# Performance work log

Measured on AMD Instinct MI355X. Metric: run time of the kernel, lower is better.

Reference implementation:

```python
import jax, jax.numpy as jnp
import numpy as np

N_NODES = 100000
N_EDGES = 1600000
N_GRAPHS = 1024
EMB = 32
HID = 64
N_CLASSES = 10
N_SHAPE = 16
N_COLOR = 8


def setup_inputs() -> dict:
    key = jax.random.key(0)
    ks = jax.random.split(key, 12)
    shape_id = jax.random.randint(ks[0], (N_NODES,), 0, N_SHAPE + 1, dtype=jnp.int32)
    color_id = jax.random.randint(ks[1], (N_NODES,), 0, N_COLOR + 1, dtype=jnp.int32)
    edge_index = jax.random.randint(ks[2], (2, N_EDGES), 0, N_NODES, dtype=jnp.int32)
    batch = jnp.sort(jax.random.randint(ks[3], (N_NODES,), 0, N_GRAPHS, dtype=jnp.int32))
    shape_table = jax.random.normal(ks[4], (N_SHAPE + 1, EMB), jnp.float32)
    color_table = jax.random.normal(ks[5], (N_COLOR + 1, EMB), jnp.float32)
    W1 = jax.random.normal(ks[6], (EMB, HID), jnp.float32) / np.sqrt(EMB)
    b1 = jnp.zeros((HID,), jnp.float32)
    W2 = jax.random.normal(ks[7], (HID, HID), jnp.float32) / np.sqrt(HID)
    b2 = jnp.zeros((HID,), jnp.float32)
    Wl = jax.random.normal(ks[8], (HID, N_CLASSES), jnp.float32) / np.sqrt(HID)
    bl = jnp.zeros((N_CLASSES,), jnp.float32)
    return dict(shape_id=shape_id, color_id=color_id, edge_index=edge_index, batch=batch,
                shape_table=shape_table, color_table=color_table,
                W1=W1, b1=b1, W2=W2, b2=b2, Wl=Wl, bl=bl)


def gcn_conv(x, W, b, src, dst, num_nodes):
    # PyG GCNConv: add self-loops, symmetric normalization D^-1/2 (A+I) D^-1/2
    h = x @ W  # [N, out]
    deg = 1.0 + jax.ops.segment_sum(jnp.ones_like(dst, jnp.float32), dst, num_segments=num_nodes)
    dis = jax.lax.rsqrt(deg)  # deg >= 1 due to self-loop
    norm = dis[src] * dis[dst]  # [E]
    agg = jax.ops.segment_sum(h[src] * norm[:, None], dst, num_segments=num_nodes)
    agg = agg + h * (dis * dis)[:, None]  # self-loop term
    return agg + b


def reference(shape_id, color_id, edge_index, batch, shape_table, color_table,
              W1, b1, W2, b2, Wl, bl):
    # padding_idx=0 -> row 0 contributes zeros
    st = shape_table.at[0].set(0.0)
    ct = color_table.at[0].set(0.0)
    x = st[shape_id] + ct[color_id]  # [N, emb]
    src, dst = edge_index[0], edge_index[1]
    x = jax.nn.relu(gcn_conv(x, W1, b1, src, dst, N_NODES))
    x = jax.nn.relu(gcn_conv(x, W2, b2, src, dst, N_NODES))
    # global_mean_pool over batch ids
    sums = jax.ops.segment_sum(x, batch, num_segments=N_GRAPHS)
    cnts = jax.ops.segment_sum(jnp.ones((x.shape[0],), x.dtype), batch, num_segments=N_GRAPHS)
    pooled = sums / jnp.maximum(cnts, 1.0)[:, None]  # [B, hidden]
    return pooled @ Wl + bl  # [B, num_classes]
```

## Files before the change

kernel.cpp:

```cpp
#include <hip/hip_runtime.h>
#include <hip/hip_bf16.h>
#include <hip/hip_fp16.h>

#define N_NODES   100000
#define N_EDGES   1600000
#define N_GRAPHS  1024
#define EMB       32
#define HID       64
#define N_CLASSES 10
#define SCAN_BLOCKS 391
#define NCOMBO 153
#define BUCK_NODES 448
#define NBUCK 224
#define BIN_CAP 8192
#define EPB 4096

typedef _Float16 f16x8 __attribute__((ext_vector_type(8)));
typedef float f32x4 __attribute__((ext_vector_type(4)));

__global__ __launch_bounds__(256) void prep_kernel(
    const int* __restrict__ sid, const int* __restrict__ cid,
    const int* __restrict__ batch, int* __restrict__ combo, int* __restrict__ gstart) {
    int v = blockIdx.x * 256 + threadIdx.x;
    if (v < N_NODES) {
        combo[v] = sid[v] * 9 + cid[v];
        int b = batch[v];
        int bp = (v == 0) ? -1 : batch[v - 1];
        for (int g = bp + 1; g <= b; ++g) gstart[g] = v;
        if (v == N_NODES - 1) {
            for (int g = b + 1; g <= N_GRAPHS; ++g) gstart[g] = N_NODES;
        }
    }
}

__global__ __launch_bounds__(64) void tc_kernel(
    const float* __restrict__ st, const float* __restrict__ ct,
    const float* __restrict__ W1, __half* __restrict__ TCh) {
    int r = blockIdx.x, j = threadIdx.x;
    int s = r / 9, c = r % 9;
    float acc = 0.0f;
    if (s != 0) {
#pragma unroll
        for (int k = 0; k < EMB; ++k) acc = fmaf(st[s * EMB + k], W1[k * HID + j], acc);
    }
    if (c != 0) {
#pragma unroll
        for (int k = 0; k < EMB; ++k) acc = fmaf(ct[c * EMB + k], W1[k * HID + j], acc);
    }
    TCh[r * HID + j] = __float2half_rn(acc);
}

__global__ __launch_bounds__(512) void binA_kernel(
    const int* __restrict__ src, const int* __restrict__ dst,
    const int* __restrict__ combo, int* __restrict__ gcur,
    int2* __restrict__ gbin) {
    __shared__ int2 stg[EPB];
    __shared__ int hist[NBUCK];
    __shared__ int base[NBUCK + 1];
    __shared__ int gstart[NBUCK];
    __shared__ int scanbuf[256];
    int t = threadIdx.x;
    int e0 = blockIdx.x * EPB;
    for (int i = t; i < NBUCK; i += 512) hist[i] = 0;
    __syncthreads();

    int2 myq[8];
    int mybo[8];
#pragma unroll
    for (int i = 0; i < 8; ++i) {
        int e = e0 + t + i * 512;
        if (e < N_EDGES) {
            int d = dst[e];
            int s = src[e];
            unsigned b = (unsigned)d / BUCK_NODES;
            int off = atomicAdd(&hist[b], 1);
            myq[i].x = s | (combo[s] << 17);
            myq[i].y = d;
            mybo[i] = (int)(b << 16) | off;
        } else {
            mybo[i] = -1;
        }
    }
    __syncthreads();

    int h = (t < NBUCK) ? hist[t] : 0;
    if (t < 256) scanbuf[t] = h;
    __syncthreads();
#pragma unroll
    for (int off = 1; off < 256; off <<= 1) {
        int x = (t < 256 && t >= off) ? scanbuf[t - off] : 0;
        __syncthreads();
        if (t < 256) scanbuf[t] += x;
        __syncthreads();
    }
    if (t < NBUCK) base[t] = scanbuf[t] - h;
    if (t == 0) base[NBUCK] = scanbuf[255];
    __syncthreads();
#pragma unroll
    for (int i = 0; i < 8; ++i) {
        if (mybo[i] >= 0) {
            int b = mybo[i] >> 16, off = mybo[i] & 0xFFFF;
            stg[base[b] + off] = myq[i];
        }
    }
    if (t < NBUCK) {
        int n = hist[t];
        gstart[t] = n ? atomicAdd(&gcur[t], n) : 0;
    }
    __syncthreads();
    int total = base[NBUCK];
    for (int i = t; i < total; i += 512) {
        int2 q = stg[i];
        unsigned b = (unsigned)q.y / BUCK_NODES;
        gbin[(size_t)b * BIN_CAP + gstart[b] + (i - base[b])] = q;
    }
}

__global__ __launch_bounds__(256) void bscan_kernel(const int* __restrict__ gcur,
                                                    int* __restrict__ bktbase) {
    __shared__ int s[256];
    int t = threadIdx.x;
    int g = (t < NBUCK) ? gcur[t] : 0;
    s[t] = g; __syncthreads();
#pragma unroll
    for (int off = 1; off < 256; off <<= 1) {
        int x = (t >= off) ? s[t - off] : 0;
        __syncthreads();
        s[t] += x;
        __syncthreads();
    }
    if (t < NBUCK) bktbase[t] = s[t] - g;
}

__global__ __launch_bounds__(512) void bucket_kernel(
    const int2* __restrict__ gbin, const int* __restrict__ gcur,
    const int* __restrict__ bktbase, float* __restrict__ dis,
    int* __restrict__ rowptr) {
    __shared__ int ldeg[BUCK_NODES];
    __shared__ int s[512];
    int b = blockIdx.x, t = threadIdx.x;
    for (int i = t; i < BUCK_NODES; i += 512) ldeg[i] = 0;
    __syncthreads();
    int n = gcur[b];
    const int2* mybin = gbin + (size_t)b * BIN_CAP;
    for (int i = t; i < n; i += 512)
        atomicAdd(&ldeg[mybin[i].y - b * BUCK_NODES], 1);
    __syncthreads();
    int d = (t < BUCK_NODES) ? ldeg[t] : 0;
    int v = b * BUCK_NODES + t;
    if (t < BUCK_NODES && v < N_NODES) dis[v] = rsqrtf(1.0f + (float)d);
    s[t] = d;
    __syncthreads();
#pragma unroll
    for (int off = 1; off < 512; off <<= 1) {
        int x = (t >= off) ? s[t - off] : 0;
        __syncthreads();
        s[t] += x;
        __syncthreads();
    }
    if (t < BUCK_NODES && v < N_NODES) rowptr[v] = bktbase[b] + s[t] - d;
    if (b == 0 && t == 0) rowptr[N_NODES] = N_EDGES;
}

__global__ __launch_bounds__(1024) void binB_kernel(
    const int2* __restrict__ gbin, const int* __restrict__ gcur,
    const int* __restrict__ rowptr, const float* __restrict__ dis,
    int2* __restrict__ epack) {
    __shared__ int curs[BUCK_NODES];
    int b = blockIdx.x, t = threadIdx.x;
    for (int i = t; i < BUCK_NODES; i += 1024) curs[i] = 0;
    __syncthreads();
    int n = gcur[b];
    const int2* mybin = gbin + (size_t)b * BIN_CAP;
    for (int i = t; i < n; i += 1024) {
        int2 q = mybin[i];
        int local = q.y - b * BUCK_NODES;
        int r = atomicAdd(&curs[local], 1);
        unsigned sx = (unsigned)q.x;
        int srci = (int)(sx & 0x1FFFF);
        int comboOff = (int)((sx >> 17) * 128u);
        int2 rec;
        rec.x = (srci << 15) | comboOff;
        rec.y = __float_as_int(dis[srci]);
        epack[rowptr[q.y] + r] = rec;
    }
}

#define AGG_CHUNK(Q, LBASE, J0)                                                \
    _Pragma("unroll")                                                          \
    for (int i = 0; i < 8; ++i) {                                              \
        int off = __builtin_amdgcn_readlane((Q).x, (LBASE) + i) & 0x7FFF;      \
        int wb  = __builtin_amdgcn_readlane((Q).y, (LBASE) + i);               \
        off = ((J0) + i < cnt) ? off : 0;                                      \
        wb  = ((J0) + i < cnt) ? wb  : 0;                                      \
        __half tv = *(const __half*)((const char*)TCs + (off + lane2));        \
        acc = fmaf(__int_as_float(wb), __half2float(tv), acc);                 \
    }

#define AGG_NODE(N, RS, RE, DV, CO)                                            \
    {                                                                          \
        int deg = (RE) - (RS);                                                 \
        int cnt = deg > 32 ? 32 : deg;                                         \
        float acc = 0.0f;                                                      \
        AGG_CHUNK(q1, (N)*16, 0)                                               \
        if (cnt > 8)  { AGG_CHUNK(q1, (N)*16 + 8, 8) }                         \
        if (cnt > 16) { AGG_CHUNK(q2, (N)*16, 16) }                            \
        if (cnt > 24) { AGG_CHUNK(q2, (N)*16 + 8, 24) }                        \
        if (deg > 32) {                                                        \
            for (int e = (RS) + 32; e < (RE); ++e) {                           \
                int2 q = epack[e];                                             \
                __half tv = *(const __half*)((const char*)TCs +                \
                                             ((q.x & 0x7FFF) + lane2));        \
                acc = fmaf(__int_as_float(q.y), __half2float(tv), acc);        \
            }                                                                  \
        }                                                                      \
        __half hv = *(const __half*)((const char*)TCs + ((CO) + lane2));       \
        float val = (DV) * fmaf(__half2float(hv), (DV), acc) + bias;           \
        val = val > 0.0f ? val : 0.0f;                                         \
        xsA[w * 4 + (N)][lane] = __float2half_rn(val * (DV));                  \
    }

__global__ __launch_bounds__(256, 6) void agg1_mm2_kernel(
    const int2* __restrict__ epack, const int* __restrict__ rowptr,
    const int* __restrict__ combo, const float* __restrict__ dis,
    const __half* __restrict__ TCh, const float* __restrict__ W2,
    const float* __restrict__ b1, __half* __restrict__ h2s) {
    __shared__ __align__(16) __half TCs[NCOMBO * HID];
    __shared__ __align__(16) __half xsA[16][72];
    __shared__ __align__(16) __half Dst[16 * 64];
    int t = threadIdx.x;
    int lane = t & 63, w = t >> 6;
    int lane2 = lane * 2;
    int vb = blockIdx.x * 16;
    int v0 = vb + w * 4;

    int sub = lane >> 4, sl = lane & 15;
    int rb = rowptr[v0 + sub];
    int2 q1 = epack[rb + sl];
    int2 q2 = epack[rb + 16 + sl];

    int r0 = __builtin_amdgcn_readfirstlane(rowptr[v0]);
    int r1 = __builtin_amdgcn_readfirstlane(rowptr[v0 + 1]);
    int r2 = __builtin_amdgcn_readfirstlane(rowptr[v0 + 2]);
    int r3 = __builtin_amdgcn_readfirstlane(rowptr[v0 + 3]);
    int r4 = __builtin_amdgcn_readfirstlane(rowptr[v0 + 4]);

    float d0 = dis[v0], d1 = dis[v0 + 1], d2 = dis[v0 + 2], d3 = dis[v0 + 3];
    int o0 = combo[v0] << 7, o1 = combo[v0 + 1] << 7;
    int o2 = combo[v0 + 2] << 7, o3 = combo[v0 + 3] << 7;
    float bias = b1[lane];

    f16x8 bf0, bf1;
    {
        int colw = (w << 4) + (lane & 15);
        int kb = (lane >> 4) * 8;
#pragma unroll
        for (int i = 0; i < 8; ++i) {
            bf0[i] = (_Float16)W2[(kb + i) * HID + colw];
            bf1[i] = (_Float16)W2[(32 + kb + i) * HID + colw];
        }
    }

    {
        const int4* s4 = (const int4*)TCh;
        int4* dd4 = (int4*)TCs;
        for (int i = t; i < NCOMBO * HID * 2 / 16; i += 256) dd4[i] = s4[i];
    }
    __syncthreads();

    AGG_NODE(0, r0, r1, d0, o0)
    AGG_NODE(1, r1, r2, d1, o1)
    AGG_NODE(2, r2, r3, d2, o2)
    AGG_NODE(3, r3, r4, d3, o3)

    __syncthreads();

    const __half* xa = &xsA[lane & 15][0];
    f16x8 a0 = *(const f16x8*)(xa + (lane >> 4) * 8);
    f16x8 a1 = *(const f16x8*)(xa + 32 + (lane >> 4) * 8);
    f32x4 dacc = {0.0f, 0.0f, 0.0f, 0.0f};
    dacc = __builtin_amdgcn_mfma_f32_16x16x32_f16(a0, bf0, dacc, 0, 0, 0);
    dacc = __builtin_amdgcn_mfma_f32_16x16x32_f16(a1, bf1, dacc, 0, 0, 0);

    {
        int colg = (w << 4) + (lane & 15);
#pragma unroll
        for (int i = 0; i < 4; ++i)
            Dst[((lane >> 4) * 4 + i) * 64 + colg] = __float2half_rn(dacc[i]);
    }
    __syncthreads();

    {
        const uint2* ds2 = (const uint2*)Dst;
        uint2* go = (uint2*)(h2s + (size_t)vb * HID);
        go[t] = ds2[t];
    }
}

__device__ __forceinline__ float agg2_node(const int* __restrict__ epackx, int sx,
                                           int rs, int re, int lane, int lane2,
                                           const __half* __restrict__ h2s) {
    float acc = 0.0f;
    int p = rs;
    for (;;) {
        int avail = re - p;
        int cnt = avail > 64 ? 64 : avail;
        int vo = (int)((((unsigned)sx) >> 15) << 7);
        int j = 0;
        for (; j + 8 <= cnt; j += 8) {
            float g[8];
#pragma unroll
            for (int i = 0; i < 8; ++i) {
                int off = __builtin_amdgcn_readlane(vo, j + i);
                g[i] = __half2float(*(const __half*)((const char*)h2s + (off + lane2)));
            }
#pragma unroll
            for (int i = 0; i < 8; ++i) acc += g[i];
        }
        if (j < cnt) {
#pragma unroll
            for (int i = 0; i < 8; ++i) {
                int jj = j + i;
                int off = __builtin_amdgcn_readlane(vo, jj & 63);
                float gv = __half2float(*(const __half*)((const char*)h2s + (off + lane2)));
                acc += (jj < cnt) ? gv : 0.0f;
            }
        }
        p += 64;
        if (p >= re) break;
        int idx = p + lane;
        idx = idx < N_EDGES ? idx : N_EDGES - 1;
        sx = epackx[idx * 2];
    }
    return acc;
}

__global__ __launch_bounds__(256, 8) void agg2_pool_kernel(
    const int2* __restrict__ epack, const int* __restrict__ rowptr,
    const __half* __restrict__ h2s, const float* __restrict__ dis,
    const float* __restrict__ b2, const int* __restrict__ batch,
    float* __restrict__ pooled) {
    int t = threadIdx.x, lane = t & 63, w = t >> 6;
    int lane2 = lane * 2;
    const int* epackx = (const int*)epack;
    int v0 = (blockIdx.x * 4 + w) * 4;

    int r0 = __builtin_amdgcn_readfirstlane(rowptr[v0]);
    int r1 = __builtin_amdgcn_readfirstlane(rowptr[v0 + 1]);
    int r2 = __builtin_amdgcn_readfirstlane(rowptr[v0 + 2]);
    int r3 = __builtin_amdgcn_readfirstlane(rowptr[v0 + 3]);
    int r4 = __builtin_amdgcn_readfirstlane(rowptr[v0 + 4]);

    int ia = r0 + lane; ia = ia < N_EDGES ? ia : N_EDGES - 1;
    int ib = r1 + lane; ib = ib < N_EDGES ? ib : N_EDGES - 1;
    int ic = r2 + lane; ic = ic < N_EDGES ? ic : N_EDGES - 1;
    int id = r3 + lane; id = id < N_EDGES ? id : N_EDGES - 1;
    int sa = epackx[ia * 2];
    int sb = epackx[ib * 2];
    int sc = epackx[ic * 2];
    int sd = epackx[id * 2];

    float bv = b2[lane];
    float acc0 = agg2_node(epackx, sa, r0, r1, lane, lane2, h2s);
    float acc1 = agg2_node(epackx, sb, r1, r2, lane, lane2, h2s);
    float acc2 = agg2_node(epackx, sc, r2, r3, lane, lane2, h2s);
    float acc3 = agg2_node(epackx, sd, r3, r4, lane, lane2, h2s);

#define AGG2_VAL(V, ACC, OUT)                                                  \
    {                                                                          \
        float dv = dis[V];                                                     \
        float self = __half2float(h2s[(size_t)(V) * HID + lane]);              \
        float val = dv * ((ACC) + self) + bv;                                  \
        OUT = val > 0.0f ? val : 0.0f;                                         \
    }
    float val0, val1, val2, val3;
    AGG2_VAL(v0, acc0, val0)
    AGG2_VAL(v0 + 1, acc1, val1)
    AGG2_VAL(v0 + 2, acc2, val2)
    AGG2_VAL(v0 + 3, acc3, val3)
#undef AGG2_VAL

    int g0 = __builtin_amdgcn_readfirstlane(batch[v0]);
    int g1 = __builtin_amdgcn_readfirstlane(batch[v0 + 1]);
    int g2 = __builtin_amdgcn_readfirstlane(batch[v0 + 2]);
    int g3 = __builtin_amdgcn_readfirstlane(batch[v0 + 3]);
    float s = val0; int g = g0;
    if (g1 == g) { s += val1; } else { unsafeAtomicAdd(&pooled[g * HID + lane], s); g = g1; s = val1; }
    if (g2 == g) { s += val2; } else { unsafeAtomicAdd(&pooled[g * HID + lane], s); g = g2; s = val2; }
    if (g3 == g) { s += val3; } else { unsafeAtomicAdd(&pooled[g * HID + lane], s); g = g3; s = val3; }
    unsafeAtomicAdd(&pooled[g * HID + lane], s);
}

__global__ __launch_bounds__(64) void logits_kernel(
    const float* __restrict__ pooled, const int* __restrict__ gstart,
    const float* __restrict__ Wl, const float* __restrict__ bl,
    float* __restrict__ out) {
    __shared__ float row[HID];
    int g = blockIdx.x, t = threadIdx.x;
    int c = gstart[g + 1] - gstart[g]; if (c < 1) c = 1;
    row[t] = pooled[g * HID + t] / (float)c;
    __syncthreads();
    if (t < N_CLASSES) {
        float acc = bl[t];
#pragma unroll
        for (int k = 0; k < HID; ++k) acc = fmaf(row[k], Wl[k * N_CLASSES + t], acc);
        out[g * N_CLASSES + t] = acc;
    }
}

extern "C" void kernel_launch(void* const* d_in, const int* in_sizes, int n_in,
                              void* d_out, int out_size, void* d_ws, size_t ws_size,
                              hipStream_t stream) {
    const int*   shape_id = (const int*)d_in[0];
    const int*   color_id = (const int*)d_in[1];
    const int*   edge_idx = (const int*)d_in[2];
    const int*   batch    = (const int*)d_in[3];
    const float* st       = (const float*)d_in[4];
    const float* ct       = (const float*)d_in[5];
    const float* W1       = (const float*)d_in[6];
    const float* b1       = (const float*)d_in[7];
    const float* W2       = (const float*)d_in[8];
    const float* b2       = (const float*)d_in[9];
    const float* Wl       = (const float*)d_in[10];
    const float* bl       = (const float*)d_in[11];
    float* out = (float*)d_out;

    const int* src = edge_idx;
    const int* dst = edge_idx + N_EDGES;

    char* ws = (char*)d_ws;
    int*    combo   = (int*)   (ws + 0);
    float*  dis     = (float*) (ws + 400384);
    int*    bktbase = (int*)   (ws + 800768);
    int*    gstart  = (int*)   (ws + 801792);
    int*    rowptr  = (int*)   (ws + 1201152);
    __half* TCh     = (__half*)(ws + 1603584);
    float*  pooled  = (float*) (ws + 1623552);
    int*    gcur    = (int*)   (ws + 1889792);
    int2*   epack   = (int2*)  (ws + 1890816);
    int2*   gbin    = (int2*)  (ws + 14690816);
    __half* h2s     = (__half*)(ws + 29370880);

    hipMemsetAsync(pooled, 0, N_GRAPHS * HID * sizeof(float), stream);
    hipMemsetAsync(gcur, 0, NBUCK * sizeof(int), stream);

    prep_kernel<<<SCAN_BLOCKS, 256, 0, stream>>>(shape_id, color_id, batch, combo, gstart);

    tc_kernel<<<NCOMBO, 64, 0, stream>>>(st, ct, W1, TCh);

    binA_kernel<<<(N_EDGES + EPB - 1) / EPB, 512, 0, stream>>>(src, dst, combo, gcur, gbin);

    bscan_kernel<<<1, 256, 0, stream>>>(gcur, bktbase);

    bucket_kernel<<<NBUCK, 512, 0, stream>>>(gbin, gcur, bktbase, dis, rowptr);

    binB_kernel<<<NBUCK, 1024, 0, stream>>>(gbin, gcur, rowptr, dis, epack);

    agg1_mm2_kernel<<<6250, 256, 0, stream>>>(epack, rowptr, combo, dis, TCh, W2, b1, h2s);

    agg2_pool_kernel<<<6250, 256, 0, stream>>>(epack, rowptr, h2s, dis, b2, batch, pooled);

    logits_kernel<<<N_GRAPHS, 64, 0, stream>>>(pooled, gstart, Wl, bl, out);
}
```

Baseline: 200.3 us.

## Split edge bins into SoA, fold bucket scan into bucket kernel, pair agg2 nodes

After: 205.2 us. +2.4%, slower.

```diff
diff --git a/kernel.cpp b/kernel.cpp
--- a/kernel.cpp
+++ b/kernel.cpp
@@ -53,7 +53,7 @@
 __global__ __launch_bounds__(512) void binA_kernel(
     const int* __restrict__ src, const int* __restrict__ dst,
     const int* __restrict__ combo, int* __restrict__ gcur,
-    int2* __restrict__ gbin) {
+    int* __restrict__ gbinx, int* __restrict__ gbiny) {
     __shared__ int2 stg[EPB];
     __shared__ int hist[NBUCK];
     __shared__ int base[NBUCK + 1];
@@ -112,39 +112,34 @@
     for (int i = t; i < total; i += 512) {
         int2 q = stg[i];
         unsigned b = (unsigned)q.y / BUCK_NODES;
-        gbin[(size_t)b * BIN_CAP + gstart[b] + (i - base[b])] = q;
-    }
-}
-
-__global__ __launch_bounds__(256) void bscan_kernel(const int* __restrict__ gcur,
-                                                    int* __restrict__ bktbase) {
-    __shared__ int s[256];
-    int t = threadIdx.x;
-    int g = (t < NBUCK) ? gcur[t] : 0;
-    s[t] = g; __syncthreads();
-#pragma unroll
-    for (int off = 1; off < 256; off <<= 1) {
-        int x = (t >= off) ? s[t - off] : 0;
-        __syncthreads();
-        s[t] += x;
-        __syncthreads();
-    }
-    if (t < NBUCK) bktbase[t] = s[t] - g;
+        size_t pos = (size_t)b * BIN_CAP + gstart[b] + (i - base[b]);
+        gbinx[pos] = q.x;
+        gbiny[pos] = q.y;
+    }
 }
 
 __global__ __launch_bounds__(512) void bucket_kernel(
-    const int2* __restrict__ gbin, const int* __restrict__ gcur,
-    const int* __restrict__ bktbase, float* __restrict__ dis,
-    int* __restrict__ rowptr) {
+    const int* __restrict__ gbiny, const int* __restrict__ gcur,
+    float* __restrict__ dis, int* __restrict__ rowptr) {
     __shared__ int ldeg[BUCK_NODES];
     __shared__ int s[512];
+    __shared__ int sc[256];
     int b = blockIdx.x, t = threadIdx.x;
+    if (t < 256) sc[t] = (t < NBUCK) ? gcur[t] : 0;
     for (int i = t; i < BUCK_NODES; i += 512) ldeg[i] = 0;
     __syncthreads();
+#pragma unroll
+    for (int off = 1; off < 256; off <<= 1) {
+        int x = (t < 256 && t >= off) ? sc[t - off] : 0;
+        __syncthreads();
+        if (t < 256) sc[t] += x;
+        __syncthreads();
+    }
+    int bb = (b == 0) ? 0 : sc[b - 1];
     int n = gcur[b];
-    const int2* mybin = gbin + (size_t)b * BIN_CAP;
+    const int* mybin = gbiny + (size_t)b * BIN_CAP;
     for (int i = t; i < n; i += 512)
-        atomicAdd(&ldeg[mybin[i].y - b * BUCK_NODES], 1);
+        atomicAdd(&ldeg[mybin[i] - b * BUCK_NODES], 1);
     __syncthreads();
     int d = (t < BUCK_NODES) ? ldeg[t] : 0;
     int v = b * BUCK_NODES + t;
@@ -158,12 +153,13 @@
         s[t] += x;
         __syncthreads();
     }
-    if (t < BUCK_NODES && v < N_NODES) rowptr[v] = bktbase[b] + s[t] - d;
+    if (t < BUCK_NODES && v < N_NODES) rowptr[v] = bb + s[t] - d;
     if (b == 0 && t == 0) rowptr[N_NODES] = N_EDGES;
 }
 
 __global__ __launch_bounds__(1024) void binB_kernel(
-    const int2* __restrict__ gbin, const int* __restrict__ gcur,
+    const int* __restrict__ gbinx, const int* __restrict__ gbiny,
+    const int* __restrict__ gcur,
     const int* __restrict__ rowptr, const float* __restrict__ dis,
     int2* __restrict__ epack) {
     __shared__ int curs[BUCK_NODES];
@@ -171,18 +167,20 @@
     for (int i = t; i < BUCK_NODES; i += 1024) curs[i] = 0;
     __syncthreads();
     int n = gcur[b];
-    const int2* mybin = gbin + (size_t)b * BIN_CAP;
+    const int* mx = gbinx + (size_t)b * BIN_CAP;
+    const int* my = gbiny + (size_t)b * BIN_CAP;
     for (int i = t; i < n; i += 1024) {
-        int2 q = mybin[i];
-        int local = q.y - b * BUCK_NODES;
+        int qx = mx[i];
+        int qy = my[i];
+        int local = qy - b * BUCK_NODES;
         int r = atomicAdd(&curs[local], 1);
-        unsigned sx = (unsigned)q.x;
+        unsigned sx = (unsigned)qx;
         int srci = (int)(sx & 0x1FFFF);
         int comboOff = (int)((sx >> 17) * 128u);
         int2 rec;
         rec.x = (srci << 15) | comboOff;
         rec.y = __float_as_int(dis[srci]);
-        epack[rowptr[q.y] + r] = rec;
+        epack[rowptr[qy] + r] = rec;
     }
 }
 
@@ -297,45 +295,58 @@
     }
 }
 
-__device__ __forceinline__ float agg2_node(const int* __restrict__ epackx, int sx,
-                                           int rs, int re, int lane, int lane2,
-                                           const __half* __restrict__ h2s) {
-    float acc = 0.0f;
-    int p = rs;
-    for (;;) {
-        int avail = re - p;
-        int cnt = avail > 64 ? 64 : avail;
-        int vo = (int)((((unsigned)sx) >> 15) << 7);
-        int j = 0;
-        for (; j + 8 <= cnt; j += 8) {
-            float g[8];
+__device__ __forceinline__ void agg2_pair(
+    const int* __restrict__ epackx, const __half* __restrict__ h2s,
+    int sxA, int rsA, int reA, int sxB, int rsB, int reB,
+    int lane2, float* outA, float* outB) {
+    int degA = reA - rsA, degB = reB - rsB;
+    int cntA = degA > 64 ? 64 : degA;
+    int cntB = degB > 64 ? 64 : degB;
+    int voA = (int)(((unsigned)sxA >> 15) << 7);
+    int voB = (int)(((unsigned)sxB >> 15) << 7);
+    float aA = 0.0f, aB = 0.0f;
+    int cmax = cntA > cntB ? cntA : cntB;
+    for (int j = 0; j < cmax; j += 8) {
+        float gA[8], gB[8];
+        bool dA = j < cntA, dB = j < cntB;
+        if (dA) {
 #pragma unroll
             for (int i = 0; i < 8; ++i) {
-                int off = __builtin_amdgcn_readlane(vo, j + i);
-                g[i] = __half2float(*(const __half*)((const char*)h2s + (off + lane2)));
+                int off = __builtin_amdgcn_readlane(voA, (j + i) & 63);
+                float v = __half2float(*(const __half*)((const char*)h2s + (off + lane2)));
+                gA[i] = (j + i < cntA) ? v : 0.0f;
             }
-#pragma unroll
-            for (int i = 0; i < 8; ++i) acc += g[i];
-        }
-        if (j < cnt) {
+        }
+        if (dB) {
 #pragma unroll
             for (int i = 0; i < 8; ++i) {
-                int jj = j + i;
-                int off = __builtin_amdgcn_readlane(vo, jj & 63);
-                float gv = __half2float(*(const __half*)((const char*)h2s + (off + lane2)));
-                acc += (jj < cnt) ? gv : 0.0f;
+                int off = __builtin_amdgcn_readlane(voB, (j + i) & 63);
+                float v = __half2float(*(const __half*)((const char*)h2s + (off + lane2)));
+                gB[i] = (j + i < cntB) ? v : 0.0f;
             }
         }
-        p += 64;
-        if (p >= re) break;
-        int idx = p + lane;
-        idx = idx < N_EDGES ? idx : N_EDGES - 1;
-        sx = epackx[idx * 2];
-    }
-    return acc;
-}
-
-__global__ __launch_bounds__(256, 8) void agg2_pool_kernel(
+        if (dA) {
+#pragma unroll
+            for (int i = 0; i < 8; ++i) aA += gA[i];
+        }
+        if (dB) {
+#pragma unroll
+            for (int i = 0; i < 8; ++i) aB += gB[i];
+        }
+    }
+    for (int e = rsA + 64; e < reA; ++e) {
+        int off = (int)(((unsigned)epackx[e * 2] >> 15) << 7);
+        aA += __half2float(*(const __half*)((const char*)h2s + (off + lane2)));
+    }
+    for (int e = rsB + 64; e < reB; ++e) {
+        int off = (int)(((unsigned)epackx[e * 2] >> 15) << 7);
+        aB += __half2float(*(const __half*)((const char*)h2s + (off + lane2)));
+    }
+    *outA = aA;
+    *outB = aB;
+}
+
+__global__ __launch_bounds__(256, 6) void agg2_pool_kernel(
     const int2* __restrict__ epack, const int* __restrict__ rowptr,
     const __half* __restrict__ h2s, const float* __restrict__ dis,
     const float* __restrict__ b2, const int* __restrict__ batch,
@@ -361,10 +372,9 @@
     int sd = epackx[id * 2];
 
     float bv = b2[lane];
-    float acc0 = agg2_node(epackx, sa, r0, r1, lane, lane2, h2s);
-    float acc1 = agg2_node(epackx, sb, r1, r2, lane, lane2, h2s);
-    float acc2 = agg2_node(epackx, sc, r2, r3, lane, lane2, h2s);
-    float acc3 = agg2_node(epackx, sd, r3, r4, lane, lane2, h2s);
+    float acc0, acc1, acc2, acc3;
+    agg2_pair(epackx, h2s, sa, r0, r1, sb, r1, r2, lane2, &acc0, &acc1);
+    agg2_pair(epackx, h2s, sc, r2, r3, sd, r3, r4, lane2, &acc2, &acc3);
 
 #define AGG2_VAL(V, ACC, OUT)                                                  \
     {                                                                          \
@@ -431,14 +441,14 @@
     char* ws = (char*)d_ws;
     int*    combo   = (int*)   (ws + 0);
     float*  dis     = (float*) (ws + 400384);
-    int*    bktbase = (int*)   (ws + 800768);
     int*    gstart  = (int*)   (ws + 801792);
     int*    rowptr  = (int*)   (ws + 1201152);
     __half* TCh     = (__half*)(ws + 1603584);
     float*  pooled  = (float*) (ws + 1623552);
     int*    gcur    = (int*)   (ws + 1889792);
     int2*   epack   = (int2*)  (ws + 1890816);
-    int2*   gbin    = (int2*)  (ws + 14690816);
+    int*    gbinx   = (int*)   (ws + 14690816);
+    int*    gbiny   = (int*)   (ws + 22030848);
     __half* h2s     = (__half*)(ws + 29370880);
 
     hipMemsetAsync(pooled, 0, N_GRAPHS * HID * sizeof(float), stream);
@@ -448,13 +458,12 @@
 
     tc_kernel<<<NCOMBO, 64, 0, stream>>>(st, ct, W1, TCh);
 
-    binA_kernel<<<(N_EDGES + EPB - 1) / EPB, 512, 0, stream>>>(src, dst, combo, gcur, gbin);
-
-    bscan_kernel<<<1, 256, 0, stream>>>(gcur, bktbase);
-
-    bucket_kernel<<<NBUCK, 512, 0, stream>>>(gbin, gcur, bktbase, dis, rowptr);
-
-    binB_kernel<<<NBUCK, 1024, 0, stream>>>(gbin, gcur, rowptr, dis, epack);
+    binA_kernel<<<(N_EDGES + EPB - 1) / EPB, 512, 0, stream>>>(src, dst, combo, gcur,
+                                                               gbinx, gbiny);
+
+    bucket_kernel<<<NBUCK, 512, 0, stream>>>(gbiny, gcur, dis, rowptr);
+
+    binB_kernel<<<NBUCK, 1024, 0, stream>>>(gbinx, gbiny, gcur, rowptr, dis, epack);
 
     agg1_mm2_kernel<<<6250, 256, 0, stream>>>(epack, rowptr, combo, dis, TCh, W2, b1, h2s);
 
```

## Fold memsets, tc and bscan into neighbouring kernels; split bin into SoA

Applied to the files above, without the earlier changes.

Result: no change. 196.7 us (-1.8%).

```diff
diff --git a/kernel.cpp b/kernel.cpp
--- a/kernel.cpp
+++ b/kernel.cpp
@@ -20,8 +20,14 @@
 
 __global__ __launch_bounds__(256) void prep_kernel(
     const int* __restrict__ sid, const int* __restrict__ cid,
-    const int* __restrict__ batch, int* __restrict__ combo, int* __restrict__ gstart) {
-    int v = blockIdx.x * 256 + threadIdx.x;
+    const int* __restrict__ batch, int* __restrict__ combo, int* __restrict__ gstart,
+    const float* __restrict__ st, const float* __restrict__ ct,
+    const float* __restrict__ W1, __half* __restrict__ TCh,
+    float* __restrict__ pooled, int* __restrict__ gcur) {
+    int t = threadIdx.x;
+    int v = blockIdx.x * 256 + t;
+    if (v < N_GRAPHS * HID) pooled[v] = 0.0f;
+    if (blockIdx.x == 0 && t < NBUCK) gcur[t] = 0;
     if (v < N_NODES) {
         combo[v] = sid[v] * 9 + cid[v];
         int b = batch[v];
@@ -31,29 +37,26 @@
             for (int g = b + 1; g <= N_GRAPHS; ++g) gstart[g] = N_NODES;
         }
     }
-}
-
-__global__ __launch_bounds__(64) void tc_kernel(
-    const float* __restrict__ st, const float* __restrict__ ct,
-    const float* __restrict__ W1, __half* __restrict__ TCh) {
-    int r = blockIdx.x, j = threadIdx.x;
-    int s = r / 9, c = r % 9;
-    float acc = 0.0f;
-    if (s != 0) {
-#pragma unroll
-        for (int k = 0; k < EMB; ++k) acc = fmaf(st[s * EMB + k], W1[k * HID + j], acc);
-    }
-    if (c != 0) {
-#pragma unroll
-        for (int k = 0; k < EMB; ++k) acc = fmaf(ct[c * EMB + k], W1[k * HID + j], acc);
-    }
-    TCh[r * HID + j] = __float2half_rn(acc);
+    if (blockIdx.x < NCOMBO && t >= 64 && t < 128) {
+        int r = blockIdx.x, j = t - 64;
+        int s = r / 9, c = r % 9;
+        float acc = 0.0f;
+        if (s != 0) {
+#pragma unroll
+            for (int k = 0; k < EMB; ++k) acc = fmaf(st[s * EMB + k], W1[k * HID + j], acc);
+        }
+        if (c != 0) {
+#pragma unroll
+            for (int k = 0; k < EMB; ++k) acc = fmaf(ct[c * EMB + k], W1[k * HID + j], acc);
+        }
+        TCh[r * HID + j] = __float2half_rn(acc);
+    }
 }
 
 __global__ __launch_bounds__(512) void binA_kernel(
     const int* __restrict__ src, const int* __restrict__ dst,
     const int* __restrict__ combo, int* __restrict__ gcur,
-    int2* __restrict__ gbin) {
+    int* __restrict__ gbinx, int* __restrict__ gbiny) {
     __shared__ int2 stg[EPB];
     __shared__ int hist[NBUCK];
     __shared__ int base[NBUCK + 1];
@@ -112,39 +115,34 @@
     for (int i = t; i < total; i += 512) {
         int2 q = stg[i];
         unsigned b = (unsigned)q.y / BUCK_NODES;
-        gbin[(size_t)b * BIN_CAP + gstart[b] + (i - base[b])] = q;
-    }
-}
-
-__global__ __launch_bounds__(256) void bscan_kernel(const int* __restrict__ gcur,
-                                                    int* __restrict__ bktbase) {
-    __shared__ int s[256];
-    int t = threadIdx.x;
-    int g = (t < NBUCK) ? gcur[t] : 0;
-    s[t] = g; __syncthreads();
-#pragma unroll
-    for (int off = 1; off < 256; off <<= 1) {
-        int x = (t >= off) ? s[t - off] : 0;
-        __syncthreads();
-        s[t] += x;
-        __syncthreads();
-    }
-    if (t < NBUCK) bktbase[t] = s[t] - g;
+        size_t pos = (size_t)b * BIN_CAP + gstart[b] + (i - base[b]);
+        gbinx[pos] = q.x;
+        gbiny[pos] = q.y;
+    }
 }
 
 __global__ __launch_bounds__(512) void bucket_kernel(
-    const int2* __restrict__ gbin, const int* __restrict__ gcur,
-    const int* __restrict__ bktbase, float* __restrict__ dis,
-    int* __restrict__ rowptr) {
+    const int* __restrict__ gbiny, const int* __restrict__ gcur,
+    float* __restrict__ dis, int* __restrict__ rowptr) {
     __shared__ int ldeg[BUCK_NODES];
     __shared__ int s[512];
+    __shared__ int sc[256];
     int b = blockIdx.x, t = threadIdx.x;
+    if (t < 256) sc[t] = (t < NBUCK) ? gcur[t] : 0;
     for (int i = t; i < BUCK_NODES; i += 512) ldeg[i] = 0;
     __syncthreads();
+#pragma unroll
+    for (int off = 1; off < 256; off <<= 1) {
+        int x = (t < 256 && t >= off) ? sc[t - off] : 0;
+        __syncthreads();
+        if (t < 256) sc[t] += x;
+        __syncthreads();
+    }
+    int bb = (b == 0) ? 0 : sc[b - 1];
     int n = gcur[b];
-    const int2* mybin = gbin + (size_t)b * BIN_CAP;
+    const int* mybin = gbiny + (size_t)b * BIN_CAP;
     for (int i = t; i < n; i += 512)
-        atomicAdd(&ldeg[mybin[i].y - b * BUCK_NODES], 1);
+        atomicAdd(&ldeg[mybin[i] - b * BUCK_NODES], 1);
     __syncthreads();
     int d = (t < BUCK_NODES) ? ldeg[t] : 0;
     int v = b * BUCK_NODES + t;
@@ -158,12 +156,13 @@
         s[t] += x;
         __syncthreads();
     }
-    if (t < BUCK_NODES && v < N_NODES) rowptr[v] = bktbase[b] + s[t] - d;
+    if (t < BUCK_NODES && v < N_NODES) rowptr[v] = bb + s[t] - d;
     if (b == 0 && t == 0) rowptr[N_NODES] = N_EDGES;
 }
 
 __global__ __launch_bounds__(1024) void binB_kernel(
-    const int2* __restrict__ gbin, const int* __restrict__ gcur,
+    const int* __restrict__ gbinx, const int* __restrict__ gbiny,
+    const int* __restrict__ gcur,
     const int* __restrict__ rowptr, const float* __restrict__ dis,
     int2* __restrict__ epack) {
     __shared__ int curs[BUCK_NODES];
@@ -171,18 +170,20 @@
     for (int i = t; i < BUCK_NODES; i += 1024) curs[i] = 0;
     __syncthreads();
     int n = gcur[b];
-    const int2* mybin = gbin + (size_t)b * BIN_CAP;
+    const int* mx = gbinx + (size_t)b * BIN_CAP;
+    const int* my = gbiny + (size_t)b * BIN_CAP;
     for (int i = t; i < n; i += 1024) {
-        int2 q = mybin[i];
-        int local = q.y - b * BUCK_NODES;
+        int qx = mx[i];
+        int qy = my[i];
+        int local = qy - b * BUCK_NODES;
         int r = atomicAdd(&curs[local], 1);
-        unsigned sx = (unsigned)q.x;
+        unsigned sx = (unsigned)qx;
         int srci = (int)(sx & 0x1FFFF);
         int comboOff = (int)((sx >> 17) * 128u);
         int2 rec;
         rec.x = (srci << 15) | comboOff;
         rec.y = __float_as_int(dis[srci]);
-        epack[rowptr[q.y] + r] = rec;
+        epack[rowptr[qy] + r] = rec;
     }
 }
 
@@ -431,30 +432,25 @@
     char* ws = (char*)d_ws;
     int*    combo   = (int*)   (ws + 0);
     float*  dis     = (float*) (ws + 400384);
-    int*    bktbase = (int*)   (ws + 800768);
     int*    gstart  = (int*)   (ws + 801792);
     int*    rowptr  = (int*)   (ws + 1201152);
     __half* TCh     = (__half*)(ws + 1603584);
     float*  pooled  = (float*) (ws + 1623552);
     int*    gcur    = (int*)   (ws + 1889792);
     int2*   epack   = (int2*)  (ws + 1890816);
-    int2*   gbin    = (int2*)  (ws + 14690816);
+    int*    gbinx   = (int*)   (ws + 14690816);
+    int*    gbiny   = (int*)   (ws + 22030848);
     __half* h2s     = (__half*)(ws + 29370880);
 
-    hipMemsetAsync(pooled, 0, N_GRAPHS * HID * sizeof(float), stream);
-    hipMemsetAsync(gcur, 0, NBUCK * sizeof(int), stream);
-
-    prep_kernel<<<SCAN_BLOCKS, 256, 0, stream>>>(shape_id, color_id, batch, combo, gstart);
-
-    tc_kernel<<<NCOMBO, 64, 0, stream>>>(st, ct, W1, TCh);
-
-    binA_kernel<<<(N_EDGES + EPB - 1) / EPB, 512, 0, stream>>>(src, dst, combo, gcur, gbin);
-
-    bscan_kernel<<<1, 256, 0, stream>>>(gcur, bktbase);
-
-    bucket_kernel<<<NBUCK, 512, 0, stream>>>(gbin, gcur, bktbase, dis, rowptr);
-
-    binB_kernel<<<NBUCK, 1024, 0, stream>>>(gbin, gcur, rowptr, dis, epack);
+    prep_kernel<<<SCAN_BLOCKS, 256, 0, stream>>>(shape_id, color_id, batch, combo, gstart,
+                                                 st, ct, W1, TCh, pooled, gcur);
+
+    binA_kernel<<<(N_EDGES + EPB - 1) / EPB, 512, 0, stream>>>(src, dst, combo, gcur,
+                                                               gbinx, gbiny);
+
+    bucket_kernel<<<NBUCK, 512, 0, stream>>>(gbiny, gcur, dis, rowptr);
+
+    binB_kernel<<<NBUCK, 1024, 0, stream>>>(gbinx, gbiny, gcur, rowptr, dis, epack);
 
     agg1_mm2_kernel<<<6250, 256, 0, stream>>>(epack, rowptr, combo, dis, TCh, W2, b1, h2s);
 
```
